# Kernel tuning notes

Hardware: AMD Instinct MI355X
Metric: run time of the kernel (lower is better)

The kernel has to match this reference:

```python
import jax, jax.numpy as jnp
import numpy as np

NM, C_IN, T, V = 256, 64, 128, 21
C_OUT = 64
N_CONVS = 3  # forward only uses convs[0..2]
EPS_BN = 1e-5


def _build_edges(nm, t):
    # replicates get_hi(): 6x6 incidence (transposed), tiled over NM*T graphs
    inc = np.array([[1, 0, 0, 0, 1, 0],
                    [1, 1, 0, 0, 0, 1],
                    [1, 0, 1, 0, 0, 1],
                    [1, 0, 0, 1, 0, 0],
                    [1, 0, 0, 0, 1, 0],
                    [0, 1, 1, 0, 0, 1]], dtype=np.int64).T
    r_idx, c_idx = np.nonzero(inc)  # row-major order, matches torch nonzero
    g = nm * t                      # num_graphs
    nnz = len(r_idx)                # 14
    row = np.tile(r_idx, g) + np.repeat(np.arange(g), nnz) * 6   # targets (edge-node ids)
    col = np.tile(c_idx, g) + np.repeat(np.arange(g), nnz) * 21  # sources (vertex ids)
    return jnp.asarray(col, jnp.int32), jnp.asarray(row, jnp.int32)


def setup_inputs() -> dict:
    key = jax.random.key(0)
    ks = jax.random.split(key, 8)
    x = jax.random.normal(ks[0], (NM, C_IN, T, V), dtype=jnp.float32)
    src, dst = _build_edges(NM, T)
    s_in = 1.0 / np.sqrt(C_IN)
    s_att = 1.0 / np.sqrt(C_OUT)
    Wl = jax.random.normal(ks[1], (N_CONVS, C_OUT, C_IN), jnp.float32) * s_in
    bl = jnp.zeros((N_CONVS, C_OUT), jnp.float32)
    Wr = jax.random.normal(ks[2], (N_CONVS, C_OUT, C_IN), jnp.float32) * s_in
    br = jnp.zeros((N_CONVS, C_OUT), jnp.float32)
    att = jax.random.normal(ks[3], (N_CONVS, C_OUT), jnp.float32) * s_att
    bias = jnp.zeros((N_CONVS, C_OUT), jnp.float32)
    gamma = jnp.full((C_OUT,), 1e-6, jnp.float32)  # bn_init(self.bn, 1e-6)
    beta = jnp.zeros((C_OUT,), jnp.float32)
    return {"x": x, "src": src, "dst": dst, "Wl": Wl, "bl": bl, "Wr": Wr,
            "br": br, "att": att, "bias": bias, "gamma": gamma, "beta": beta}


def _gatv2(feat, src_all, dst_all, valid, Wl, bl, Wr, br, att, bias, n):
    # GATv2Conv, heads=1: e_ij = att . LeakyReLU(Wl x_j + Wr x_i); softmax over dst
    xl = feat @ Wl.T + bl           # [N, Cout]
    xr = feat @ Wr.T + br           # [N, Cout]
    msg = xl[src_all]               # [E, Cout]
    e = jax.nn.leaky_relu(msg + xr[dst_all], 0.2) @ att  # [E]
    e = jnp.where(valid, e, -1e9)   # removed self-loops excluded
    m = jax.ops.segment_max(e, dst_all, num_segments=n)
    a = jnp.exp(e - m[dst_all]) * valid
    denom = jax.ops.segment_sum(a, dst_all, num_segments=n)
    a = a / denom[dst_all]
    return jax.ops.segment_sum(a[:, None] * msg, dst_all, num_segments=n) + bias


def reference(x, src, dst, Wl, bl, Wr, br, att, bias, gamma, beta):
    nm, c, t, v = x.shape
    n = nm * t * v
    feat = jnp.transpose(x, (0, 2, 3, 1)).reshape(n, c)  # '(nm t v) c'
    # PyG GATv2: remove existing self-loops, then add self-loops for all N nodes
    loop = jnp.arange(n, dtype=src.dtype)
    src_all = jnp.concatenate([src, loop])
    dst_all = jnp.concatenate([dst, loop])
    valid = jnp.concatenate([src != dst, jnp.ones((n,), bool)])
    y = None
    for i in range(N_CONVS):
        z = _gatv2(feat, src_all, dst_all, valid,
                   Wl[i], bl[i], Wr[i], br[i], att[i], bias[i], n)
        y = z if y is None else y + z
    y = y.reshape(nm, C_OUT, t, v)  # matches torch .view on node-major buffer
    # BatchNorm2d (eval, running mean 0 / var 1), gamma initialized to 1e-6
    y = y / jnp.sqrt(1.0 + EPS_BN) * gamma[None, :, None, None] + beta[None, :, None, None]
    return jax.nn.relu(y + x)  # residual identity (in_channels == out_channels)
```

## Files before the change

kernel.cpp:

```cpp
#include <hip/hip_runtime.h>
#include <hip/hip_bf16.h>

#define NMSLICE 2688
#define NMELEMS 172032
#define NNODE   688128
#define NDST    196608
#define BNRS    0.9999950000374996f

typedef __attribute__((ext_vector_type(8))) _Float16 half8;
typedef __attribute__((ext_vector_type(2))) _Float16 half2v;
typedef __attribute__((ext_vector_type(4))) unsigned uintx4;
typedef __attribute__((ext_vector_type(4))) float  floatx4;

__device__ __forceinline__ short h2s(float f) {
    union { _Float16 h; short s; } c;
    c.h = (_Float16)f;
    return c.s;
}

__device__ __forceinline__ void loadrow_h(const short* buf, int row, int cb, half2v* o) {
    #pragma unroll
    for (int h = 0; h < 2; ++h) {
        const int k8 = cb * 2 + h;
        uintx4 v = *reinterpret_cast<const uintx4*>(&buf[row * 64 + ((k8 ^ (row & 7)) << 3)]);
        #pragma unroll
        for (int j = 0; j < 4; ++j) o[h * 4 + j] = __builtin_bit_cast(half2v, v[j]);
    }
}

__device__ __forceinline__ float edot2(const half2v* a, const half2v* xr, const half2v* m) {
    half2v s = { (_Float16)0, (_Float16)0 };
    const half2v c02 = { (_Float16)0.2f, (_Float16)0.2f };
    #pragma unroll
    for (int j = 0; j < 8; ++j) {
        half2v z = m[j] + xr[j];
        z = __builtin_elementwise_max(z, c02 * z);
        s += a[j] * z;
    }
    float e = (float)s[0] + (float)s[1];
    e += __shfl_xor(e, 1);
    e += __shfl_xor(e, 2);
    return e;
}

__global__ void __launch_bounds__(256) prep_weights(
    const float* __restrict__ Wl, const float* __restrict__ Wr,
    const float* __restrict__ bl, const float* __restrict__ bias,
    const float* __restrict__ att,
    short* __restrict__ wfrag, float* __restrict__ csum, float* __restrict__ bsum,
    short* __restrict__ att_h)
{
    const int task = blockIdx.x * 256 + threadIdx.x;
    const int lane = task & 63;
    const int ks   = (task >> 6) & 1;
    const int nt   = (task >> 7) & 3;
    const int m    = task >> 9;
    const int co = nt * 16 + (lane & 15);
    const int k0 = ks * 32 + (lane >> 4) * 8;
    short v[8];
    if (m < 6) {
        const int cv = m >> 1;
        const float* W = (m & 1) ? (Wr + cv * 4096) : (Wl + cv * 4096);
        #pragma unroll
        for (int j = 0; j < 8; ++j) v[j] = h2s(W[co * 64 + k0 + j]);
    } else {
        #pragma unroll
        for (int j = 0; j < 8; ++j)
            v[j] = h2s(Wl[co*64 + k0 + j] + Wl[4096 + co*64 + k0 + j] + Wl[8192 + co*64 + k0 + j]);
    }
    #pragma unroll
    for (int j = 0; j < 8; ++j) wfrag[task * 8 + j] = v[j];
    if (blockIdx.x == 0 && threadIdx.x < 192) {
        const int t = threadIdx.x;
        att_h[t] = h2s(att[t]);
        if (t < 64) {
            csum[t] = bl[t] + bl[64+t] + bl[128+t] + bias[t] + bias[64+t] + bias[128+t];
            bsum[t] = bias[t] + bias[64+t] + bias[128+t];
        }
    }
}

__global__ void __launch_bounds__(256) gat_heavy(
    const float* __restrict__ x,
    const short* __restrict__ wfrag,
    const float* __restrict__ bl, const float* __restrict__ br,
    const short* __restrict__ att_h, const float* __restrict__ bsum,
    const float* __restrict__ gamma, const float* __restrict__ beta,
    float* __restrict__ out)
{
    __shared__ short F [4 * 24 * 64];
    __shared__ short XL[4 * 24 * 64];
    __shared__ short XR[4 * 12 * 64];

    const int lane = threadIdx.x & 63;
    const int wave = threadIdx.x >> 6;
    const int sbid = ((blockIdx.x & 7) << 9) + (blockIdx.x >> 3);
    const int W  = sbid * 4 + wave;
    const int n0 = W * 12;
    const int s0 = W * 42;

    short* Fw  = F  + wave * (24 * 64);
    short* XLw = XL + wave * (24 * 64);
    short* XRw = XR + wave * (12 * 64);

    const int nmD = n0 / NMSLICE, rmD = n0 - nmD * NMSLICE;
    const int nmS = s0 / NMSLICE, rmS = s0 - nmS * NMSLICE;

    #pragma unroll
    for (int i = 0; i < 3; ++i) {
        const int task = i * 64 + lane;
        const int r  = task % 24;
        const int k8 = task / 24;
        const float* bp;
        if (r < 12) {
            bp = x + (size_t)nmD * NMELEMS + rmD + r;
        } else {
            const int s = r - 12;
            const int gl = s >= 6 ? 1 : 0;
            bp = x + (size_t)nmS * NMELEMS + rmS + gl * 21 + (s - gl * 6);
        }
        short v[8];
        #pragma unroll
        for (int j = 0; j < 8; ++j) v[j] = h2s(bp[(size_t)(k8 * 8 + j) * NMSLICE]);
        *reinterpret_cast<half8*>(&Fw[r * 64 + ((k8 ^ (r & 7)) << 3)]) =
            *reinterpret_cast<half8*>(v);
    }

    const int l15 = lane & 15, l4 = lane >> 4;
    const int nd = lane >> 2, cb = lane & 3;
    const bool act = nd < 12;
    const int gl2 = nd >= 6 ? 1 : 0;
    const int rr = nd - gl2 * 6;
    const int srow = 12 + gl2 * 6;
    const unsigned long long TBL =
        31ull | (34ull << 8) | (36ull << 16) | (8ull << 24) | (17ull << 32) | (38ull << 40);
    unsigned mask = (unsigned)((TBL >> (rr * 8)) & 63u);
    if (W == 0 && gl2 == 0) mask &= ~(1u << rr);

    float yacc[16];
    #pragma unroll
    for (int j = 0; j < 16; ++j) yacc[j] = 0.f;

    for (int cv = 0; cv < 3; ++cv) {
        #pragma unroll
        for (int nt = 0; nt < 4; ++nt) {
            const int co = nt * 16 + l15;
            const short* wbL = wfrag + (size_t)(((cv * 2    ) * 4 + nt) * 2) * 512;
            const short* wbR = wfrag + (size_t)(((cv * 2 + 1) * 4 + nt) * 2) * 512;
            half8 wl0 = *reinterpret_cast<const half8*>(wbL + lane * 8);
            half8 wl1 = *reinterpret_cast<const half8*>(wbL + 512 + lane * 8);
            half8 wr0 = *reinterpret_cast<const half8*>(wbR + lane * 8);
            half8 wr1 = *reinterpret_cast<const half8*>(wbR + 512 + lane * 8);
            const float biL = bl[cv * 64 + co];
            const float biR = br[cv * 64 + co];
            #pragma unroll
            for (int u = 0; u < 3; ++u) {
                const int mt = (u == 1) ? 1 : 0;
                const int arow = mt * 16 + l15;
                const float bi = (u == 2) ? biR : biL;
                floatx4 acc = { bi, bi, bi, bi };
                half8 b0 = (u == 2) ? wr0 : wl0;
                half8 b1 = (u == 2) ? wr1 : wl1;
                half8 a0 = *reinterpret_cast<const half8*>(
                    &Fw[arow * 64 + ((l4 ^ (arow & 7)) << 3)]);
                half8 a1 = *reinterpret_cast<const half8*>(
                    &Fw[arow * 64 + (((4 + l4) ^ (arow & 7)) << 3)]);
                acc = __builtin_amdgcn_mfma_f32_16x16x32_f16(a0, b0, acc, 0, 0, 0);
                acc = __builtin_amdgcn_mfma_f32_16x16x32_f16(a1, b1, acc, 0, 0, 0);
                short* dstb = (u == 2) ? XRw : XLw;
                const int rlim = (u == 2) ? 12 : 24;
                #pragma unroll
                for (int qq = 0; qq < 4; ++qq) {
                    const int row = mt * 16 + l4 * 4 + qq;
                    if (row < rlim)
                        dstb[row * 64 + (((co >> 3) ^ (row & 7)) << 3) + (co & 7)] = h2s(acc[qq]);
                }
            }
        }

        if (act) {
            half2v a2[8], xr2[8], m2[8], o2[8];
            {
                const uintx4* ap = reinterpret_cast<const uintx4*>(att_h + cv * 64 + cb * 16);
                uintx4 v0 = ap[0], v1 = ap[1];
                #pragma unroll
                for (int j = 0; j < 4; ++j) {
                    a2[j]     = __builtin_bit_cast(half2v, v0[j]);
                    a2[4 + j] = __builtin_bit_cast(half2v, v1[j]);
                }
            }
            loadrow_h(XRw, nd, cb, xr2);
            loadrow_h(XLw, nd, cb, m2);
            float e = edot2(a2, xr2, m2);
            float w = __expf(e);
            float denom = w;
            half2v w2 = { (_Float16)w, (_Float16)w };
            #pragma unroll
            for (int j = 0; j < 8; ++j) o2[j] = w2 * m2[j];
            #pragma unroll
            for (int c = 0; c < 6; ++c) {
                loadrow_h(XLw, srow + c, cb, m2);
                e = edot2(a2, xr2, m2);
                w = (mask & (1u << c)) ? __expf(e) : 0.f;
                denom += w;
                w2[0] = (_Float16)w; w2[1] = (_Float16)w;
                #pragma unroll
                for (int j = 0; j < 8; ++j) o2[j] += w2 * m2[j];
            }
            const float inv = 1.0f / denom;
            #pragma unroll
            for (int j = 0; j < 8; ++j) {
                yacc[2*j]   = fmaf((float)o2[j][0], inv, yacc[2*j]);
                yacc[2*j+1] = fmaf((float)o2[j][1], inv, yacc[2*j+1]);
            }
        }
    }

    if (act) {
        const size_t i0 = (size_t)(n0 + nd) * 64 + cb * 16;
        const int cobn = ((rmD + nd) * 64 + cb * 16) / NMSLICE;
        const float sc = gamma[cobn] * BNRS;
        const float bt = beta[cobn];
        #pragma unroll
        for (int j4 = 0; j4 < 4; ++j4) {
            floatx4 xv = *reinterpret_cast<const floatx4*>(x + i0 + j4 * 4);
            floatx4 ov;
            #pragma unroll
            for (int j = 0; j < 4; ++j) {
                float val = fmaf(yacc[j4 * 4 + j] + bsum[cb * 16 + j4 * 4 + j], sc, bt) + xv[j];
                ov[j] = fmaxf(val, 0.f);
            }
            *reinterpret_cast<floatx4*>(out + i0 + j4 * 4) = ov;
        }
    }
}

__global__ void __launch_bounds__(256) gat_light(
    const float* __restrict__ x,
    const short* __restrict__ wfrag,
    const float* __restrict__ csum,
    const float* __restrict__ gamma, const float* __restrict__ beta,
    float* __restrict__ out)
{
    __shared__ short F[256 * 64];

    const int t  = threadIdx.x;
    const int n0 = NDST + blockIdx.x * 256;

    {
        const int node = n0 + t;
        const int nm = node / NMSLICE;
        const int rm = node - nm * NMSLICE;
        const float* bp = x + (size_t)nm * NMELEMS + rm;
        #pragma unroll
        for (int k8 = 0; k8 < 8; ++k8) {
            short v[8];
            #pragma unroll
            for (int j = 0; j < 8; ++j) v[j] = h2s(bp[(size_t)(k8 * 8 + j) * NMSLICE]);
            *reinterpret_cast<half8*>(&F[t * 64 + ((k8 ^ (t & 7)) << 3)]) =
                *reinterpret_cast<half8*>(v);
        }
    }
    __syncthreads();

    const int wave = t >> 6, lane = t & 63;
    const int l15 = lane & 15, l4 = lane >> 4;
    const int rm0 = n0 % NMSLICE;
    #pragma unroll
    for (int ti = 0; ti < 16; ++ti) {
        const int tile = wave * 16 + ti;
        const int mt = tile >> 2, nt = tile & 3;
        const int co = nt * 16 + l15;
        const float bi = csum[co];
        floatx4 acc = { bi, bi, bi, bi };
        const short* wbase = wfrag + (size_t)((6 * 4 + nt) * 2) * 512;
        const int arow = mt * 16 + l15;
        #pragma unroll
        for (int ks = 0; ks < 2; ++ks) {
            half8 bfr = *reinterpret_cast<const half8*>(wbase + ks * 512 + lane * 8);
            const int k8 = ks * 4 + l4;
            half8 afr = *reinterpret_cast<const half8*>(
                &F[arow * 64 + ((k8 ^ (arow & 7)) << 3)]);
            acc = __builtin_amdgcn_mfma_f32_16x16x32_f16(afr, bfr, acc, 0, 0, 0);
        }
        #pragma unroll
        for (int qq = 0; qq < 4; ++qq) {
            const int row = mt * 16 + l4 * 4 + qq;
            int rm = rm0 + row; if (rm >= NMSLICE) rm -= NMSLICE;
            const int cobn = (rm * 64 + co) / NMSLICE;
            const size_t fi = (size_t)(n0 + row) * 64 + co;
            const float val = fmaf(acc[qq], gamma[cobn] * BNRS, beta[cobn]) + x[fi];
            out[fi] = fmaxf(val, 0.f);
        }
    }
}

extern "C" void kernel_launch(void* const* d_in, const int* in_sizes, int n_in,
                              void* d_out, int out_size, void* d_ws, size_t ws_size,
                              hipStream_t stream) {
    const float* x     = (const float*)d_in[0];
    const float* Wl    = (const float*)d_in[3];
    const float* bl    = (const float*)d_in[4];
    const float* Wr    = (const float*)d_in[5];
    const float* br    = (const float*)d_in[6];
    const float* att   = (const float*)d_in[7];
    const float* bias  = (const float*)d_in[8];
    const float* gamma = (const float*)d_in[9];
    const float* beta  = (const float*)d_in[10];
    float* out = (float*)d_out;

    short* wfrag = (short*)d_ws;
    float* csum  = (float*)((char*)d_ws + 57344);
    float* bsum  = csum + 64;
    short* att_h = (short*)(bsum + 64);

    hipLaunchKernelGGL(prep_weights, dim3(14), dim3(256), 0, stream,
                       Wl, Wr, bl, bias, att, wfrag, csum, bsum, att_h);
    hipLaunchKernelGGL(gat_heavy, dim3(4096), dim3(256), 0, stream,
                       x, wfrag, bl, br, att_h, bsum, gamma, beta, out);
    hipLaunchKernelGGL(gat_light, dim3(1920), dim3(256), 0, stream,
                       x, wfrag, csum, gamma, beta, out);
}
```

Before: 178.9 us.

## Fuse heavy and light GAT kernels, load A fragments directly into registers

```diff
diff --git a/kernel.cpp b/kernel.cpp
--- a/kernel.cpp
+++ b/kernel.cpp
@@ -41,6 +41,13 @@
     e += __shfl_xor(e, 1);
     e += __shfl_xor(e, 2);
     return e;
+}
+
+__device__ __forceinline__ half8 loadfrag(const float* bp, int k0) {
+    half8 v;
+    #pragma unroll
+    for (int j = 0; j < 8; ++j) v[j] = (_Float16)bp[(size_t)(k0 + j) * NMSLICE];
+    return v;
 }
 
 __global__ void __launch_bounds__(256) prep_weights(
@@ -80,217 +87,192 @@
     }
 }
 
-__global__ void __launch_bounds__(256) gat_heavy(
+__global__ void __launch_bounds__(256) gat_fused(
     const float* __restrict__ x,
     const short* __restrict__ wfrag,
     const float* __restrict__ bl, const float* __restrict__ br,
     const short* __restrict__ att_h, const float* __restrict__ bsum,
-    const float* __restrict__ gamma, const float* __restrict__ beta,
-    float* __restrict__ out)
-{
-    __shared__ short F [4 * 24 * 64];
-    __shared__ short XL[4 * 24 * 64];
-    __shared__ short XR[4 * 12 * 64];
-
-    const int lane = threadIdx.x & 63;
-    const int wave = threadIdx.x >> 6;
-    const int sbid = ((blockIdx.x & 7) << 9) + (blockIdx.x >> 3);
-    const int W  = sbid * 4 + wave;
-    const int n0 = W * 12;
-    const int s0 = W * 42;
-
-    short* Fw  = F  + wave * (24 * 64);
-    short* XLw = XL + wave * (24 * 64);
-    short* XRw = XR + wave * (12 * 64);
-
-    const int nmD = n0 / NMSLICE, rmD = n0 - nmD * NMSLICE;
-    const int nmS = s0 / NMSLICE, rmS = s0 - nmS * NMSLICE;
-
-    #pragma unroll
-    for (int i = 0; i < 3; ++i) {
-        const int task = i * 64 + lane;
-        const int r  = task % 24;
-        const int k8 = task / 24;
-        const float* bp;
-        if (r < 12) {
-            bp = x + (size_t)nmD * NMELEMS + rmD + r;
-        } else {
-            const int s = r - 12;
-            const int gl = s >= 6 ? 1 : 0;
-            bp = x + (size_t)nmS * NMELEMS + rmS + gl * 21 + (s - gl * 6);
-        }
-        short v[8];
-        #pragma unroll
-        for (int j = 0; j < 8; ++j) v[j] = h2s(bp[(size_t)(k8 * 8 + j) * NMSLICE]);
-        *reinterpret_cast<half8*>(&Fw[r * 64 + ((k8 ^ (r & 7)) << 3)]) =
-            *reinterpret_cast<half8*>(v);
-    }
-
-    const int l15 = lane & 15, l4 = lane >> 4;
-    const int nd = lane >> 2, cb = lane & 3;
-    const bool act = nd < 12;
-    const int gl2 = nd >= 6 ? 1 : 0;
-    const int rr = nd - gl2 * 6;
-    const int srow = 12 + gl2 * 6;
-    const unsigned long long TBL =
-        31ull | (34ull << 8) | (36ull << 16) | (8ull << 24) | (17ull << 32) | (38ull << 40);
-    unsigned mask = (unsigned)((TBL >> (rr * 8)) & 63u);
-    if (W == 0 && gl2 == 0) mask &= ~(1u << rr);
-
-    float yacc[16];
-    #pragma unroll
-    for (int j = 0; j < 16; ++j) yacc[j] = 0.f;
-
-    for (int cv = 0; cv < 3; ++cv) {
-        #pragma unroll
-        for (int nt = 0; nt < 4; ++nt) {
-            const int co = nt * 16 + l15;
-            const short* wbL = wfrag + (size_t)(((cv * 2    ) * 4 + nt) * 2) * 512;
-            const short* wbR = wfrag + (size_t)(((cv * 2 + 1) * 4 + nt) * 2) * 512;
-            half8 wl0 = *reinterpret_cast<const half8*>(wbL + lane * 8);
-            half8 wl1 = *reinterpret_cast<const half8*>(wbL + 512 + lane * 8);
-            half8 wr0 = *reinterpret_cast<const half8*>(wbR + lane * 8);
-            half8 wr1 = *reinterpret_cast<const half8*>(wbR + 512 + lane * 8);
-            const float biL = bl[cv * 64 + co];
-            const float biR = br[cv * 64 + co];
-            #pragma unroll
-            for (int u = 0; u < 3; ++u) {
-                const int mt = (u == 1) ? 1 : 0;
-                const int arow = mt * 16 + l15;
-                const float bi = (u == 2) ? biR : biL;
-                floatx4 acc = { bi, bi, bi, bi };
-                half8 b0 = (u == 2) ? wr0 : wl0;
-                half8 b1 = (u == 2) ? wr1 : wl1;
-                half8 a0 = *reinterpret_cast<const half8*>(
-                    &Fw[arow * 64 + ((l4 ^ (arow & 7)) << 3)]);
-                half8 a1 = *reinterpret_cast<const half8*>(
-                    &Fw[arow * 64 + (((4 + l4) ^ (arow & 7)) << 3)]);
-                acc = __builtin_amdgcn_mfma_f32_16x16x32_f16(a0, b0, acc, 0, 0, 0);
-                acc = __builtin_amdgcn_mfma_f32_16x16x32_f16(a1, b1, acc, 0, 0, 0);
-                short* dstb = (u == 2) ? XRw : XLw;
-                const int rlim = (u == 2) ? 12 : 24;
-                #pragma unroll
-                for (int qq = 0; qq < 4; ++qq) {
-                    const int row = mt * 16 + l4 * 4 + qq;
-                    if (row < rlim)
-                        dstb[row * 64 + (((co >> 3) ^ (row & 7)) << 3) + (co & 7)] = h2s(acc[qq]);
-                }
-            }
-        }
-
-        if (act) {
-            half2v a2[8], xr2[8], m2[8], o2[8];
-            {
-                const uintx4* ap = reinterpret_cast<const uintx4*>(att_h + cv * 64 + cb * 16);
-                uintx4 v0 = ap[0], v1 = ap[1];
-                #pragma unroll
-                for (int j = 0; j < 4; ++j) {
-                    a2[j]     = __builtin_bit_cast(half2v, v0[j]);
-                    a2[4 + j] = __builtin_bit_cast(half2v, v1[j]);
-                }
-            }
-            loadrow_h(XRw, nd, cb, xr2);
-            loadrow_h(XLw, nd, cb, m2);
-            float e = edot2(a2, xr2, m2);
-            float w = __expf(e);
-            float denom = w;
-            half2v w2 = { (_Float16)w, (_Float16)w };
-            #pragma unroll
-            for (int j = 0; j < 8; ++j) o2[j] = w2 * m2[j];
-            #pragma unroll
-            for (int c = 0; c < 6; ++c) {
-                loadrow_h(XLw, srow + c, cb, m2);
-                e = edot2(a2, xr2, m2);
-                w = (mask & (1u << c)) ? __expf(e) : 0.f;
-                denom += w;
-                w2[0] = (_Float16)w; w2[1] = (_Float16)w;
-                #pragma unroll
-                for (int j = 0; j < 8; ++j) o2[j] += w2 * m2[j];
-            }
-            const float inv = 1.0f / denom;
-            #pragma unroll
-            for (int j = 0; j < 8; ++j) {
-                yacc[2*j]   = fmaf((float)o2[j][0], inv, yacc[2*j]);
-                yacc[2*j+1] = fmaf((float)o2[j][1], inv, yacc[2*j+1]);
-            }
-        }
-    }
-
-    if (act) {
-        const size_t i0 = (size_t)(n0 + nd) * 64 + cb * 16;
-        const int cobn = ((rmD + nd) * 64 + cb * 16) / NMSLICE;
-        const float sc = gamma[cobn] * BNRS;
-        const float bt = beta[cobn];
-        #pragma unroll
-        for (int j4 = 0; j4 < 4; ++j4) {
-            floatx4 xv = *reinterpret_cast<const floatx4*>(x + i0 + j4 * 4);
-            floatx4 ov;
-            #pragma unroll
-            for (int j = 0; j < 4; ++j) {
-                float val = fmaf(yacc[j4 * 4 + j] + bsum[cb * 16 + j4 * 4 + j], sc, bt) + xv[j];
-                ov[j] = fmaxf(val, 0.f);
-            }
-            *reinterpret_cast<floatx4*>(out + i0 + j4 * 4) = ov;
-        }
-    }
-}
-
-__global__ void __launch_bounds__(256) gat_light(
-    const float* __restrict__ x,
-    const short* __restrict__ wfrag,
     const float* __restrict__ csum,
     const float* __restrict__ gamma, const float* __restrict__ beta,
     float* __restrict__ out)
 {
-    __shared__ short F[256 * 64];
-
-    const int t  = threadIdx.x;
-    const int n0 = NDST + blockIdx.x * 256;
-
-    {
-        const int node = n0 + t;
-        const int nm = node / NMSLICE;
-        const int rm = node - nm * NMSLICE;
-        const float* bp = x + (size_t)nm * NMELEMS + rm;
-        #pragma unroll
-        for (int k8 = 0; k8 < 8; ++k8) {
-            short v[8];
+    __shared__ short XL[4 * 24 * 64];
+    __shared__ short XR[4 * 12 * 64];
+
+    const int lane = threadIdx.x & 63;
+    const int wave = threadIdx.x >> 6;
+    const int l15 = lane & 15, l4 = lane >> 4;
+    const int g47 = blockIdx.x / 47;
+    const int i47 = blockIdx.x - g47 * 47;
+
+    if (i47 < 32) {
+        const int W  = (g47 * 32 + i47) * 4 + wave;
+        const int n0 = W * 12;
+        const int s0 = W * 42;
+        short* XLw = XL + wave * (24 * 64);
+        short* XRw = XR + wave * (12 * 64);
+
+        const int nmD = n0 / NMSLICE, rmD = n0 - nmD * NMSLICE;
+        const int nmS = s0 / NMSLICE, rmS = s0 - nmS * NMSLICE;
+
+        auto rowptr = [&](int r) -> const float* {
+            if (r >= 24) r -= 24;
+            if (r < 12) return x + (size_t)nmD * NMELEMS + rmD + r;
+            const int s = r - 12;
+            const int gl = s >= 6 ? 1 : 0;
+            return x + (size_t)nmS * NMELEMS + rmS + gl * 21 + (s - gl * 6);
+        };
+        const float* p0 = rowptr(l15);
+        const float* p1 = rowptr(16 + l15);
+        half8 aA[2][2];
+        aA[0][0] = loadfrag(p0, l4 * 8);
+        aA[0][1] = loadfrag(p0, 32 + l4 * 8);
+        aA[1][0] = loadfrag(p1, l4 * 8);
+        aA[1][1] = loadfrag(p1, 32 + l4 * 8);
+
+        const int nd = lane >> 2, cb = lane & 3;
+        const bool act = nd < 12;
+        const int gl2 = nd >= 6 ? 1 : 0;
+        const int rr = nd - gl2 * 6;
+        const int srow = 12 + gl2 * 6;
+        const unsigned long long TBL =
+            31ull | (34ull << 8) | (36ull << 16) | (8ull << 24) | (17ull << 32) | (38ull << 40);
+        unsigned mask = (unsigned)((TBL >> (rr * 8)) & 63u);
+        if (W == 0 && gl2 == 0) mask &= ~(1u << rr);
+
+        float yacc[16];
+        #pragma unroll
+        for (int j = 0; j < 16; ++j) yacc[j] = 0.f;
+
+        for (int cv = 0; cv < 3; ++cv) {
             #pragma unroll
-            for (int j = 0; j < 8; ++j) v[j] = h2s(bp[(size_t)(k8 * 8 + j) * NMSLICE]);
-            *reinterpret_cast<half8*>(&F[t * 64 + ((k8 ^ (t & 7)) << 3)]) =
-                *reinterpret_cast<half8*>(v);
-        }
-    }
-    __syncthreads();
-
-    const int wave = t >> 6, lane = t & 63;
-    const int l15 = lane & 15, l4 = lane >> 4;
-    const int rm0 = n0 % NMSLICE;
-    #pragma unroll
-    for (int ti = 0; ti < 16; ++ti) {
-        const int tile = wave * 16 + ti;
-        const int mt = tile >> 2, nt = tile & 3;
-        const int co = nt * 16 + l15;
-        const float bi = csum[co];
-        floatx4 acc = { bi, bi, bi, bi };
-        const short* wbase = wfrag + (size_t)((6 * 4 + nt) * 2) * 512;
-        const int arow = mt * 16 + l15;
-        #pragma unroll
-        for (int ks = 0; ks < 2; ++ks) {
-            half8 bfr = *reinterpret_cast<const half8*>(wbase + ks * 512 + lane * 8);
-            const int k8 = ks * 4 + l4;
-            half8 afr = *reinterpret_cast<const half8*>(
-                &F[arow * 64 + ((k8 ^ (arow & 7)) << 3)]);
-            acc = __builtin_amdgcn_mfma_f32_16x16x32_f16(afr, bfr, acc, 0, 0, 0);
-        }
-        #pragma unroll
-        for (int qq = 0; qq < 4; ++qq) {
-            const int row = mt * 16 + l4 * 4 + qq;
-            int rm = rm0 + row; if (rm >= NMSLICE) rm -= NMSLICE;
-            const int cobn = (rm * 64 + co) / NMSLICE;
-            const size_t fi = (size_t)(n0 + row) * 64 + co;
-            const float val = fmaf(acc[qq], gamma[cobn] * BNRS, beta[cobn]) + x[fi];
-            out[fi] = fmaxf(val, 0.f);
+            for (int nt = 0; nt < 4; ++nt) {
+                const int co = nt * 16 + l15;
+                const short* wbL = wfrag + (size_t)(((cv * 2    ) * 4 + nt) * 2) * 512;
+                const short* wbR = wfrag + (size_t)(((cv * 2 + 1) * 4 + nt) * 2) * 512;
+                half8 wl0 = *reinterpret_cast<const half8*>(wbL + lane * 8);
+                half8 wl1 = *reinterpret_cast<const half8*>(wbL + 512 + lane * 8);
+                half8 wr0 = *reinterpret_cast<const half8*>(wbR + lane * 8);
+                half8 wr1 = *reinterpret_cast<const half8*>(wbR + 512 + lane * 8);
+                const float biL = bl[cv * 64 + co];
+                const float biR = br[cv * 64 + co];
+                #pragma unroll
+                for (int u = 0; u < 3; ++u) {
+                    const int mt = (u == 1) ? 1 : 0;
+                    const float bi = (u == 2) ? biR : biL;
+                    floatx4 acc = { bi, bi, bi, bi };
+                    acc = __builtin_amdgcn_mfma_f32_16x16x32_f16(
+                        aA[mt][0], (u == 2) ? wr0 : wl0, acc, 0, 0, 0);
+                    acc = __builtin_amdgcn_mfma_f32_16x16x32_f16(
+                        aA[mt][1], (u == 2) ? wr1 : wl1, acc, 0, 0, 0);
+                    short* dstb = (u == 2) ? XRw : XLw;
+                    const int rlim = (u == 2) ? 12 : 24;
+                    #pragma unroll
+                    for (int qq = 0; qq < 4; ++qq) {
+                        const int row = mt * 16 + l4 * 4 + qq;
+                        if (row < rlim)
+                            dstb[row * 64 + (((co >> 3) ^ (row & 7)) << 3) + (co & 7)] = h2s(acc[qq]);
+                    }
+                }
+            }
+
+            if (act) {
+                half2v a2[8], xr2[8], m2[8], o2[8];
+                {
+                    const uintx4* ap = reinterpret_cast<const uintx4*>(att_h + cv * 64 + cb * 16);
+                    uintx4 v0 = ap[0], v1 = ap[1];
+                    #pragma unroll
+                    for (int j = 0; j < 4; ++j) {
+                        a2[j]     = __builtin_bit_cast(half2v, v0[j]);
+                        a2[4 + j] = __builtin_bit_cast(half2v, v1[j]);
+                    }
+                }
+                loadrow_h(XRw, nd, cb, xr2);
+                loadrow_h(XLw, nd, cb, m2);
+                float e = edot2(a2, xr2, m2);
+                float w = __expf(e);
+                float denom = w;
+                half2v w2 = { (_Float16)w, (_Float16)w };
+                #pragma unroll
+                for (int j = 0; j < 8; ++j) o2[j] = w2 * m2[j];
+                #pragma unroll
+                for (int c = 0; c < 6; ++c) {
+                    loadrow_h(XLw, srow + c, cb, m2);
+                    e = edot2(a2, xr2, m2);
+                    w = (mask & (1u << c)) ? __expf(e) : 0.f;
+                    denom += w;
+                    w2[0] = (_Float16)w; w2[1] = (_Float16)w;
+                    #pragma unroll
+                    for (int j = 0; j < 8; ++j) o2[j] += w2 * m2[j];
+                }
+                const float inv = 1.0f / denom;
+                #pragma unroll
+                for (int j = 0; j < 8; ++j) {
+                    yacc[2*j]   = fmaf((float)o2[j][0], inv, yacc[2*j]);
+                    yacc[2*j+1] = fmaf((float)o2[j][1], inv, yacc[2*j+1]);
+                }
+            }
+        }
+
+        if (act) {
+            const size_t i0 = (size_t)(n0 + nd) * 64 + cb * 16;
+            const int cobn = ((rmD + nd) * 64 + cb * 16) / NMSLICE;
+            const float sc = gamma[cobn] * BNRS;
+            const float bt = beta[cobn];
+            #pragma unroll
+            for (int j4 = 0; j4 < 4; ++j4) {
+                floatx4 xv = *reinterpret_cast<const floatx4*>(x + i0 + j4 * 4);
+                floatx4 ov;
+                #pragma unroll
+                for (int j = 0; j < 4; ++j) {
+                    float val = fmaf(yacc[j4*4+j] + bsum[cb*16 + j4*4 + j], sc, bt) + xv[j];
+                    ov[j] = fmaxf(val, 0.f);
+                }
+                *reinterpret_cast<floatx4*>(out + i0 + j4 * 4) = ov;
+            }
+        }
+    } else {
+        const int lid = g47 * 15 + (i47 - 32);
+        const int n0 = NDST + lid * 256;
+
+        half8 fA[4][2];
+        int rowbase[4];
+        #pragma unroll
+        for (int mtl = 0; mtl < 4; ++mtl) {
+            const int row = (wave * 4 + mtl) * 16 + l15;
+            const int node = n0 + row;
+            const int nm = node / NMSLICE;
+            const int rm = node - nm * NMSLICE;
+            const float* bp = x + (size_t)nm * NMELEMS + rm;
+            fA[mtl][0] = loadfrag(bp, l4 * 8);
+            fA[mtl][1] = loadfrag(bp, 32 + l4 * 8);
+            rowbase[mtl] = row;
+        }
+
+        const int rm0 = n0 % NMSLICE;
+        #pragma unroll
+        for (int nt = 0; nt < 4; ++nt) {
+            const int co = nt * 16 + l15;
+            const short* wbase = wfrag + (size_t)((6 * 4 + nt) * 2) * 512;
+            half8 w0 = *reinterpret_cast<const half8*>(wbase + lane * 8);
+            half8 w1 = *reinterpret_cast<const half8*>(wbase + 512 + lane * 8);
+            const float bi = csum[co];
+            #pragma unroll
+            for (int mtl = 0; mtl < 4; ++mtl) {
+                floatx4 acc = { bi, bi, bi, bi };
+                acc = __builtin_amdgcn_mfma_f32_16x16x32_f16(fA[mtl][0], w0, acc, 0, 0, 0);
+                acc = __builtin_amdgcn_mfma_f32_16x16x32_f16(fA[mtl][1], w1, acc, 0, 0, 0);
+                const int mrow = (wave * 4 + mtl) * 16;
+                #pragma unroll
+                for (int qq = 0; qq < 4; ++qq) {
+                    const int row = mrow + l4 * 4 + qq;
+                    int rm = rm0 + row; if (rm >= NMSLICE) rm -= NMSLICE;
+                    const int cobn = (rm * 64 + co) / NMSLICE;
+                    const size_t fi = (size_t)(n0 + row) * 64 + co;
+                    const float val = fmaf(acc[qq], gamma[cobn] * BNRS, beta[cobn]) + x[fi];
+                    out[fi] = fmaxf(val, 0.f);
+                }
+            }
         }
     }
 }
@@ -316,8 +298,6 @@
 
     hipLaunchKernelGGL(prep_weights, dim3(14), dim3(256), 0, stream,
                        Wl, Wr, bl, bias, att, wfrag, csum, bsum, att_h);
-    hipLaunchKernelGGL(gat_heavy, dim3(4096), dim3(256), 0, stream,
-                       x, wfrag, bl, br, att_h, bsum, gamma, beta, out);
-    hipLaunchKernelGGL(gat_light, dim3(1920), dim3(256), 0, stream,
-                       x, wfrag, csum, gamma, beta, out);
-}
+    hipLaunchKernelGGL(gat_fused, dim3(128 * 47), dim3(256), 0, stream,
+                       x, wfrag, bl, br, att_h, bsum, csum, gamma, beta, out);
+}
```

Result: slower. 224.8 us (+25.7%).

## Cut heavy-kernel LDS and registers to raise occupancy in gat_heavy

Applied to the files above, without the earlier changes.

```diff
diff --git a/kernel.cpp b/kernel.cpp
--- a/kernel.cpp
+++ b/kernel.cpp
@@ -80,7 +80,7 @@
     }
 }
 
-__global__ void __launch_bounds__(256) gat_heavy(
+__global__ void __launch_bounds__(256, 6) gat_heavy(
     const float* __restrict__ x,
     const short* __restrict__ wfrag,
     const float* __restrict__ bl, const float* __restrict__ br,
@@ -88,9 +88,7 @@
     const float* __restrict__ gamma, const float* __restrict__ beta,
     float* __restrict__ out)
 {
-    __shared__ short F [4 * 24 * 64];
-    __shared__ short XL[4 * 24 * 64];
-    __shared__ short XR[4 * 12 * 64];
+    __shared__ short B[4][36 * 64];
 
     const int lane = threadIdx.x & 63;
     const int wave = threadIdx.x >> 6;
@@ -99,9 +97,8 @@
     const int n0 = W * 12;
     const int s0 = W * 42;
 
-    short* Fw  = F  + wave * (24 * 64);
-    short* XLw = XL + wave * (24 * 64);
-    short* XRw = XR + wave * (12 * 64);
+    short* XLw = B[wave];
+    short* XRw = B[wave] + 24 * 64;
 
     const int nmD = n0 / NMSLICE, rmD = n0 - nmD * NMSLICE;
     const int nmS = s0 / NMSLICE, rmS = s0 - nmS * NMSLICE;
@@ -122,11 +119,22 @@
         short v[8];
         #pragma unroll
         for (int j = 0; j < 8; ++j) v[j] = h2s(bp[(size_t)(k8 * 8 + j) * NMSLICE]);
-        *reinterpret_cast<half8*>(&Fw[r * 64 + ((k8 ^ (r & 7)) << 3)]) =
+        *reinterpret_cast<half8*>(&XLw[r * 64 + ((k8 ^ (r & 7)) << 3)]) =
             *reinterpret_cast<half8*>(v);
     }
 
     const int l15 = lane & 15, l4 = lane >> 4;
+
+    half8 aA[2][2];
+    #pragma unroll
+    for (int mt = 0; mt < 2; ++mt) {
+        const int arow = mt * 16 + l15;
+        #pragma unroll
+        for (int ks = 0; ks < 2; ++ks)
+            aA[mt][ks] = *reinterpret_cast<const half8*>(
+                &B[wave][arow * 64 + (((ks * 4 + l4) ^ (arow & 7)) << 3)]);
+    }
+
     const int nd = lane >> 2, cb = lane & 3;
     const bool act = nd < 12;
     const int gl2 = nd >= 6 ? 1 : 0;
@@ -137,36 +145,25 @@
     unsigned mask = (unsigned)((TBL >> (rr * 8)) & 63u);
     if (W == 0 && gl2 == 0) mask &= ~(1u << rr);
 
-    float yacc[16];
-    #pragma unroll
-    for (int j = 0; j < 16; ++j) yacc[j] = 0.f;
+    half2v yacc2[8];
+    #pragma unroll
+    for (int j = 0; j < 8; ++j) yacc2[j] = half2v{ (_Float16)0, (_Float16)0 };
 
     for (int cv = 0; cv < 3; ++cv) {
         #pragma unroll
         for (int nt = 0; nt < 4; ++nt) {
             const int co = nt * 16 + l15;
-            const short* wbL = wfrag + (size_t)(((cv * 2    ) * 4 + nt) * 2) * 512;
-            const short* wbR = wfrag + (size_t)(((cv * 2 + 1) * 4 + nt) * 2) * 512;
-            half8 wl0 = *reinterpret_cast<const half8*>(wbL + lane * 8);
-            half8 wl1 = *reinterpret_cast<const half8*>(wbL + 512 + lane * 8);
-            half8 wr0 = *reinterpret_cast<const half8*>(wbR + lane * 8);
-            half8 wr1 = *reinterpret_cast<const half8*>(wbR + 512 + lane * 8);
-            const float biL = bl[cv * 64 + co];
-            const float biR = br[cv * 64 + co];
             #pragma unroll
             for (int u = 0; u < 3; ++u) {
                 const int mt = (u == 1) ? 1 : 0;
-                const int arow = mt * 16 + l15;
-                const float bi = (u == 2) ? biR : biL;
+                const int m = cv * 2 + (u == 2 ? 1 : 0);
+                const short* wb = wfrag + (size_t)((m * 4 + nt) * 2) * 512;
+                half8 w0 = *reinterpret_cast<const half8*>(wb + lane * 8);
+                half8 w1 = *reinterpret_cast<const half8*>(wb + 512 + lane * 8);
+                const float bi = ((u == 2) ? br : bl)[cv * 64 + co];
                 floatx4 acc = { bi, bi, bi, bi };
-                half8 b0 = (u == 2) ? wr0 : wl0;
-                half8 b1 = (u == 2) ? wr1 : wl1;
-                half8 a0 = *reinterpret_cast<const half8*>(
-                    &Fw[arow * 64 + ((l4 ^ (arow & 7)) << 3)]);
-                half8 a1 = *reinterpret_cast<const half8*>(
-                    &Fw[arow * 64 + (((4 + l4) ^ (arow & 7)) << 3)]);
-                acc = __builtin_amdgcn_mfma_f32_16x16x32_f16(a0, b0, acc, 0, 0, 0);
-                acc = __builtin_amdgcn_mfma_f32_16x16x32_f16(a1, b1, acc, 0, 0, 0);
+                acc = __builtin_amdgcn_mfma_f32_16x16x32_f16(aA[mt][0], w0, acc, 0, 0, 0);
+                acc = __builtin_amdgcn_mfma_f32_16x16x32_f16(aA[mt][1], w1, acc, 0, 0, 0);
                 short* dstb = (u == 2) ? XRw : XLw;
                 const int rlim = (u == 2) ? 12 : 24;
                 #pragma unroll
@@ -207,12 +204,10 @@
                 #pragma unroll
                 for (int j = 0; j < 8; ++j) o2[j] += w2 * m2[j];
             }
-            const float inv = 1.0f / denom;
-            #pragma unroll
-            for (int j = 0; j < 8; ++j) {
-                yacc[2*j]   = fmaf((float)o2[j][0], inv, yacc[2*j]);
-                yacc[2*j+1] = fmaf((float)o2[j][1], inv, yacc[2*j+1]);
-            }
+            const _Float16 invh = (_Float16)(1.0f / denom);
+            const half2v inv2 = { invh, invh };
+            #pragma unroll
+            for (int j = 0; j < 8; ++j) yacc2[j] += inv2 * o2[j];
         }
     }
 
@@ -227,7 +222,9 @@
             floatx4 ov;
             #pragma unroll
             for (int j = 0; j < 4; ++j) {
-                float val = fmaf(yacc[j4 * 4 + j] + bsum[cb * 16 + j4 * 4 + j], sc, bt) + xv[j];
+                const int jj = j4 * 4 + j;
+                const float yv = (float)yacc2[jj >> 1][jj & 1];
+                float val = fmaf(yv + bsum[cb * 16 + jj], sc, bt) + xv[j];
                 ov[j] = fmaxf(val, 0.f);
             }
             *reinterpret_cast<floatx4*>(out + i0 + j4 * 4) = ov;
```

Measured after the change: 234.8 us. +31.3%, slower.

## Double per-wave tile in gat_heavy, hoist A fragments into registers, drop F buffer

Applied to the files above, without the earlier changes.

```diff
diff --git a/kernel.cpp b/kernel.cpp
--- a/kernel.cpp
+++ b/kernel.cpp
@@ -88,58 +88,69 @@
     const float* __restrict__ gamma, const float* __restrict__ beta,
     float* __restrict__ out)
 {
-    __shared__ short F [4 * 24 * 64];
-    __shared__ short XL[4 * 24 * 64];
-    __shared__ short XR[4 * 12 * 64];
+    __shared__ short XL[4 * 48 * 64];
+    __shared__ short XR[4 * 24 * 64];
 
     const int lane = threadIdx.x & 63;
     const int wave = threadIdx.x >> 6;
-    const int sbid = ((blockIdx.x & 7) << 9) + (blockIdx.x >> 3);
+    const int sbid = ((blockIdx.x & 7) << 8) + (blockIdx.x >> 3);
     const int W  = sbid * 4 + wave;
-    const int n0 = W * 12;
-    const int s0 = W * 42;
-
-    short* Fw  = F  + wave * (24 * 64);
-    short* XLw = XL + wave * (24 * 64);
-    short* XRw = XR + wave * (12 * 64);
+    const int n0 = W * 24;
+    const int s0 = W * 84;
+
+    short* XLw = XL + wave * (48 * 64);
+    short* XRw = XR + wave * (24 * 64);
 
     const int nmD = n0 / NMSLICE, rmD = n0 - nmD * NMSLICE;
     const int nmS = s0 / NMSLICE, rmS = s0 - nmS * NMSLICE;
 
     #pragma unroll
-    for (int i = 0; i < 3; ++i) {
+    for (int i = 0; i < 6; ++i) {
         const int task = i * 64 + lane;
-        const int r  = task % 24;
-        const int k8 = task / 24;
+        const int r  = task % 48;
+        const int k8 = task / 48;
         const float* bp;
-        if (r < 12) {
+        if (r < 24) {
             bp = x + (size_t)nmD * NMELEMS + rmD + r;
         } else {
-            const int s = r - 12;
-            const int gl = s >= 6 ? 1 : 0;
+            const int s = r - 24, gl = s / 6;
             bp = x + (size_t)nmS * NMELEMS + rmS + gl * 21 + (s - gl * 6);
         }
         short v[8];
         #pragma unroll
         for (int j = 0; j < 8; ++j) v[j] = h2s(bp[(size_t)(k8 * 8 + j) * NMSLICE]);
-        *reinterpret_cast<half8*>(&Fw[r * 64 + ((k8 ^ (r & 7)) << 3)]) =
+        *reinterpret_cast<half8*>(&XLw[r * 64 + ((k8 ^ (r & 7)) << 3)]) =
             *reinterpret_cast<half8*>(v);
     }
 
     const int l15 = lane & 15, l4 = lane >> 4;
-    const int nd = lane >> 2, cb = lane & 3;
-    const bool act = nd < 12;
-    const int gl2 = nd >= 6 ? 1 : 0;
-    const int rr = nd - gl2 * 6;
-    const int srow = 12 + gl2 * 6;
+
+    half8 aA[3][2];
+    #pragma unroll
+    for (int t = 0; t < 3; ++t) {
+        const int arow = t * 16 + l15;
+        #pragma unroll
+        for (int ks = 0; ks < 2; ++ks)
+            aA[t][ks] = *reinterpret_cast<const half8*>(
+                &XLw[arow * 64 + (((ks * 4 + l4) ^ (arow & 7)) << 3)]);
+    }
+
+    const int ndA = lane >> 2, cbA = lane & 3;
+    const int ndB = 16 + (lane >> 2), cbB = lane & 3;
     const unsigned long long TBL =
         31ull | (34ull << 8) | (36ull << 16) | (8ull << 24) | (17ull << 32) | (38ull << 40);
-    unsigned mask = (unsigned)((TBL >> (rr * 8)) & 63u);
-    if (W == 0 && gl2 == 0) mask &= ~(1u << rr);
-
-    float yacc[16];
-    #pragma unroll
-    for (int j = 0; j < 16; ++j) yacc[j] = 0.f;
+    const int glA = ndA / 6, rrA = ndA - glA * 6, srowA = 24 + glA * 6;
+    const int glB = ndB / 6, rrB = ndB - glB * 6, srowB = 24 + glB * 6;
+    unsigned maskA = (unsigned)((TBL >> (rrA * 8)) & 63u);
+    unsigned maskB = (unsigned)((TBL >> (rrB * 8)) & 63u);
+    if (W == 0 && glA == 0) maskA &= ~(1u << rrA);
+
+    half2v yA2[8], yB2[8];
+    #pragma unroll
+    for (int j = 0; j < 8; ++j) {
+        yA2[j] = half2v{ (_Float16)0, (_Float16)0 };
+        yB2[j] = half2v{ (_Float16)0, (_Float16)0 };
+    }
 
     for (int cv = 0; cv < 3; ++cv) {
         #pragma unroll
@@ -155,33 +166,33 @@
             const float biR = br[cv * 64 + co];
             #pragma unroll
             for (int u = 0; u < 3; ++u) {
-                const int mt = (u == 1) ? 1 : 0;
-                const int arow = mt * 16 + l15;
-                const float bi = (u == 2) ? biR : biL;
-                floatx4 acc = { bi, bi, bi, bi };
-                half8 b0 = (u == 2) ? wr0 : wl0;
-                half8 b1 = (u == 2) ? wr1 : wl1;
-                half8 a0 = *reinterpret_cast<const half8*>(
-                    &Fw[arow * 64 + ((l4 ^ (arow & 7)) << 3)]);
-                half8 a1 = *reinterpret_cast<const half8*>(
-                    &Fw[arow * 64 + (((4 + l4) ^ (arow & 7)) << 3)]);
-                acc = __builtin_amdgcn_mfma_f32_16x16x32_f16(a0, b0, acc, 0, 0, 0);
-                acc = __builtin_amdgcn_mfma_f32_16x16x32_f16(a1, b1, acc, 0, 0, 0);
-                short* dstb = (u == 2) ? XRw : XLw;
-                const int rlim = (u == 2) ? 12 : 24;
+                floatx4 acc = { biL, biL, biL, biL };
+                acc = __builtin_amdgcn_mfma_f32_16x16x32_f16(aA[u][0], wl0, acc, 0, 0, 0);
+                acc = __builtin_amdgcn_mfma_f32_16x16x32_f16(aA[u][1], wl1, acc, 0, 0, 0);
                 #pragma unroll
                 for (int qq = 0; qq < 4; ++qq) {
-                    const int row = mt * 16 + l4 * 4 + qq;
-                    if (row < rlim)
-                        dstb[row * 64 + (((co >> 3) ^ (row & 7)) << 3) + (co & 7)] = h2s(acc[qq]);
+                    const int row = u * 16 + l4 * 4 + qq;
+                    XLw[row * 64 + (((co >> 3) ^ (row & 7)) << 3) + (co & 7)] = h2s(acc[qq]);
                 }
             }
-        }
-
-        if (act) {
+            #pragma unroll
+            for (int mtx = 0; mtx < 2; ++mtx) {
+                floatx4 acc = { biR, biR, biR, biR };
+                acc = __builtin_amdgcn_mfma_f32_16x16x32_f16(aA[mtx][0], wr0, acc, 0, 0, 0);
+                acc = __builtin_amdgcn_mfma_f32_16x16x32_f16(aA[mtx][1], wr1, acc, 0, 0, 0);
+                #pragma unroll
+                for (int qq = 0; qq < 4; ++qq) {
+                    const int row = mtx * 16 + l4 * 4 + qq;
+                    if (row < 24)
+                        XRw[row * 64 + (((co >> 3) ^ (row & 7)) << 3) + (co & 7)] = h2s(acc[qq]);
+                }
+            }
+        }
+
+        {
             half2v a2[8], xr2[8], m2[8], o2[8];
             {
-                const uintx4* ap = reinterpret_cast<const uintx4*>(att_h + cv * 64 + cb * 16);
+                const uintx4* ap = reinterpret_cast<const uintx4*>(att_h + cv * 64 + cbA * 16);
                 uintx4 v0 = ap[0], v1 = ap[1];
                 #pragma unroll
                 for (int j = 0; j < 4; ++j) {
@@ -189,8 +200,8 @@
                     a2[4 + j] = __builtin_bit_cast(half2v, v1[j]);
                 }
             }
-            loadrow_h(XRw, nd, cb, xr2);
-            loadrow_h(XLw, nd, cb, m2);
+            loadrow_h(XRw, ndA, cbA, xr2);
+            loadrow_h(XLw, ndA, cbA, m2);
             float e = edot2(a2, xr2, m2);
             float w = __expf(e);
             float denom = w;
@@ -199,26 +210,58 @@
             for (int j = 0; j < 8; ++j) o2[j] = w2 * m2[j];
             #pragma unroll
             for (int c = 0; c < 6; ++c) {
-                loadrow_h(XLw, srow + c, cb, m2);
+                loadrow_h(XLw, srowA + c, cbA, m2);
                 e = edot2(a2, xr2, m2);
-                w = (mask & (1u << c)) ? __expf(e) : 0.f;
+                w = (maskA & (1u << c)) ? __expf(e) : 0.f;
                 denom += w;
                 w2[0] = (_Float16)w; w2[1] = (_Float16)w;
                 #pragma unroll
                 for (int j = 0; j < 8; ++j) o2[j] += w2 * m2[j];
             }
-            const float inv = 1.0f / denom;
-            #pragma unroll
-            for (int j = 0; j < 8; ++j) {
-                yacc[2*j]   = fmaf((float)o2[j][0], inv, yacc[2*j]);
-                yacc[2*j+1] = fmaf((float)o2[j][1], inv, yacc[2*j+1]);
-            }
-        }
-    }
-
-    if (act) {
-        const size_t i0 = (size_t)(n0 + nd) * 64 + cb * 16;
-        const int cobn = ((rmD + nd) * 64 + cb * 16) / NMSLICE;
+            const _Float16 invh = (_Float16)(1.0f / denom);
+            const half2v inv2 = { invh, invh };
+            #pragma unroll
+            for (int j = 0; j < 8; ++j) yA2[j] += inv2 * o2[j];
+        }
+        if (lane < 32) {
+            half2v a2[8], xr2[8], m2[8], o2[8];
+            {
+                const uintx4* ap = reinterpret_cast<const uintx4*>(att_h + cv * 64 + cbB * 16);
+                uintx4 v0 = ap[0], v1 = ap[1];
+                #pragma unroll
+                for (int j = 0; j < 4; ++j) {
+                    a2[j]     = __builtin_bit_cast(half2v, v0[j]);
+                    a2[4 + j] = __builtin_bit_cast(half2v, v1[j]);
+                }
+            }
+            loadrow_h(XRw, ndB, cbB, xr2);
+            loadrow_h(XLw, ndB, cbB, m2);
+            float e = edot2(a2, xr2, m2);
+            float w = __expf(e);
+            float denom = w;
+            half2v w2 = { (_Float16)w, (_Float16)w };
+            #pragma unroll
+            for (int j = 0; j < 8; ++j) o2[j] = w2 * m2[j];
+            #pragma unroll
+            for (int c = 0; c < 6; ++c) {
+                loadrow_h(XLw, srowB + c, cbB, m2);
+                e = edot2(a2, xr2, m2);
+                w = (maskB & (1u << c)) ? __expf(e) : 0.f;
+                denom += w;
+                w2[0] = (_Float16)w; w2[1] = (_Float16)w;
+                #pragma unroll
+                for (int j = 0; j < 8; ++j) o2[j] += w2 * m2[j];
+            }
+            const _Float16 invh = (_Float16)(1.0f / denom);
+            const half2v inv2 = { invh, invh };
+            #pragma unroll
+            for (int j = 0; j < 8; ++j) yB2[j] += inv2 * o2[j];
+        }
+    }
+
+    {
+        const size_t i0 = (size_t)(n0 + ndA) * 64 + cbA * 16;
+        const int cobn = ((rmD + ndA) * 64 + cbA * 16) / NMSLICE;
         const float sc = gamma[cobn] * BNRS;
         const float bt = beta[cobn];
         #pragma unroll
@@ -227,7 +270,28 @@
             floatx4 ov;
             #pragma unroll
             for (int j = 0; j < 4; ++j) {
-                float val = fmaf(yacc[j4 * 4 + j] + bsum[cb * 16 + j4 * 4 + j], sc, bt) + xv[j];
+                const int jj = j4 * 4 + j;
+                const float yv = (float)yA2[jj >> 1][jj & 1];
+                float val = fmaf(yv + bsum[cbA * 16 + jj], sc, bt) + xv[j];
+                ov[j] = fmaxf(val, 0.f);
+            }
+            *reinterpret_cast<floatx4*>(out + i0 + j4 * 4) = ov;
+        }
+    }
+    if (lane < 32) {
+        const size_t i0 = (size_t)(n0 + ndB) * 64 + cbB * 16;
+        const int cobn = ((rmD + ndB) * 64 + cbB * 16) / NMSLICE;
+        const float sc = gamma[cobn] * BNRS;
+        const float bt = beta[cobn];
+        #pragma unroll
+        for (int j4 = 0; j4 < 4; ++j4) {
+            floatx4 xv = *reinterpret_cast<const floatx4*>(x + i0 + j4 * 4);
+            floatx4 ov;
+            #pragma unroll
+            for (int j = 0; j < 4; ++j) {
+                const int jj = j4 * 4 + j;
+                const float yv = (float)yB2[jj >> 1][jj & 1];
+                float val = fmaf(yv + bsum[cbB * 16 + jj], sc, bt) + xv[j];
                 ov[j] = fmaxf(val, 0.f);
             }
             *reinterpret_cast<floatx4*>(out + i0 + j4 * 4) = ov;
@@ -316,7 +380,7 @@
 
     hipLaunchKernelGGL(prep_weights, dim3(14), dim3(256), 0, stream,
                        Wl, Wr, bl, bias, att, wfrag, csum, bsum, att_h);
-    hipLaunchKernelGGL(gat_heavy, dim3(4096), dim3(256), 0, stream,
+    hipLaunchKernelGGL(gat_heavy, dim3(2048), dim3(256), 0, stream,
                        x, wfrag, bl, br, att_h, bsum, gamma, beta, out);
     hipLaunchKernelGGL(gat_light, dim3(1920), dim3(256), 0, stream,
                        x, wfrag, csum, gamma, beta, out);
```

After: 179.8 us. Within noise of the previous version (+0.5%).
